# Kernel optimization log

Measured on AMD Instinct MI355X. Metric: run time of the kernel, lower is better.

Reference implementation:

```python
import jax, jax.numpy as jnp
import numpy as np

BOUNDS = (0, 256, 384, 448, 512)  # rot_idx, trans_idx, angle_idx, embedding_dim
SCALES = [1, 2, 4, 8, 16, 32, 64]  # 2**i for i in range(scales+1), scales=6


def _pairwise_dist(q, e):
    # q: [M, C] queries, e: [K, C] codebook; per-segment squared dist / seg_dim, summed
    d = jnp.zeros((q.shape[0], e.shape[0]), dtype=q.dtype)
    for s, t in zip(BOUNDS[:-1], BOUNDS[1:]):
        qs, es = q[:, s:t], e[:, s:t]
        d = d + (jnp.sum(qs * qs, axis=1, keepdims=True)
                 + jnp.sum(es * es, axis=1)
                 - 2.0 * qs @ es.T) / (t - s)
    return d


def _elem_dist(q, k):
    # q, k: [B, C, N]; elementwise per-segment squared distance / seg_dim -> [B, N]
    d = 0.0
    for s, t in zip(BOUNDS[:-1], BOUNDS[1:]):
        diff = q[:, s:t] - k[:, s:t]
        d = d + jnp.sum(diff * diff, axis=1) / (t - s)
    return d


def _downsample_area(f, pn):
    # f: [B, C, N], pn divides N -> block-mean pooling (torch 'area')
    B, C, N = f.shape
    return f.reshape(B, C, pn, N // pn).mean(axis=-1)


def _upsample_linear(h, N):
    # h: [B, C, pn] -> [B, C, N], torch mode='linear', align_corners=False
    pn = h.shape[-1]
    src = (jnp.arange(N, dtype=jnp.float32) + 0.5) * (pn / N) - 0.5
    src = jnp.clip(src, 0.0, pn - 1)
    i0 = jnp.floor(src).astype(jnp.int32)
    i1 = jnp.minimum(i0 + 1, pn - 1)
    w = (src - i0).astype(h.dtype)
    return h[..., i0] * (1.0 - w) + h[..., i1] * w


def setup_inputs() -> dict:
    key = jax.random.key(0)
    k1, k2, k3 = jax.random.split(key, 3)
    C = 512
    f_BNC = jax.random.normal(k1, (1024, 64, C), dtype=jnp.float32)
    base = jax.random.normal(k2, (2048, C), dtype=jnp.float32)
    proj_W = jax.random.normal(k3, (C, C), dtype=jnp.float32) / np.sqrt(C)
    return {"f_BNC": f_BNC, "base": base, "proj_W": proj_W}


def reference(f_BNC, base, proj_W):
    embedding = base @ proj_W.T              # update_embedding(): proj(base)
    emb_ng = jax.lax.stop_gradient(embedding)
    f_BCN = jnp.transpose(f_BNC, (0, 2, 1))  # [B, C, N]
    B, C, N = f_BCN.shape
    f_no_grad = jax.lax.stop_gradient(f_BCN)
    f_rest = f_no_grad
    f_hat = jnp.zeros_like(f_rest)
    commit = jnp.zeros((B, N), dtype=f_BCN.dtype)
    qlat = jnp.zeros((B, N), dtype=f_BCN.dtype)
    for pn in SCALES:
        rest_NC = jnp.transpose(_downsample_area(f_rest, pn), (0, 2, 1)).reshape(-1, C)
        d = _pairwise_dist(jax.lax.stop_gradient(rest_NC), emb_ng)  # [B*pn, K]
        idx = jnp.argmin(d, axis=1)
        h_NC = embedding[idx]                                        # gather (grad -> codebook)
        h_BCn = jnp.transpose(h_NC.reshape(B, pn, C), (0, 2, 1))
        h_BCN = _upsample_linear(h_BCn, N)
        f_hat = f_hat + h_BCN
        f_rest = f_rest - h_BCN
        commit = commit + 0.25 * _elem_dist(jax.lax.stop_gradient(f_hat), f_BCN)
        qlat = qlat + _elem_dist(f_hat, f_no_grad)
    SN = float(len(SCALES))
    commit = commit / SN
    qlat = qlat / SN
    f_hat_st = jax.lax.stop_gradient(f_hat) - f_no_grad + f_BCN  # straight-through
    return (jnp.transpose(f_hat_st, (0, 2, 1)), commit, qlat)
```

## Files before the change

kernel.cpp:

```cpp
#include <hip/hip_runtime.h>

typedef __attribute__((ext_vector_type(8))) _Float16 f16x8;
typedef __attribute__((ext_vector_type(4))) float f32x4;

#define B_    1024
#define C_    512
#define NCODE 2048
#define NTOT  (B_ * 64 * C_)
#define BN_   (B_ * 64)
#define DELTA 6e-3f

__device__ __forceinline__ float wseg(int k) {
    return k < 256 ? (1.0f / 256.0f) : (k < 384 ? (1.0f / 128.0f) : (1.0f / 64.0f));
}

__device__ __forceinline__ unsigned packkey(float s, int code) {
    unsigned u = __float_as_uint(s);
    u = (u & 0x80000000u) ? ~u : (u | 0x80000000u);
    return (u & 0xFFFFF800u) | (unsigned)code;
}
__device__ __forceinline__ float unpk(unsigned k) {
    unsigned us = k & 0xFFFFF800u;
    return (us & 0x80000000u) ? __uint_as_float(us ^ 0x80000000u) : __uint_as_float(~us);
}

__global__ __launch_bounds__(256) void k_gemm_e(const float* __restrict__ A,
                                                const float* __restrict__ Bm,
                                                float* __restrict__ E) {
    __shared__ float As[16][68];
    __shared__ float Bs[16][68];
    int tid = threadIdx.x;
    int m0 = blockIdx.x * 64, n0 = blockIdx.y * 64;
    float acc[4][4] = {};
    int tx = tid & 15, ty = tid >> 4;
    int kk = tid & 15, rr = tid >> 4;
    for (int k0 = 0; k0 < 512; k0 += 16) {
        #pragma unroll
        for (int i = 0; i < 4; ++i) {
            As[kk][rr + i * 16] = A[(m0 + rr + i * 16) * 512 + k0 + kk];
            Bs[kk][rr + i * 16] = Bm[(n0 + rr + i * 16) * 512 + k0 + kk];
        }
        __syncthreads();
        #pragma unroll
        for (int k = 0; k < 16; ++k) {
            float4 a = *(const float4*)&As[k][ty * 4];
            float4 b = *(const float4*)&Bs[k][tx * 4];
            #pragma unroll
            for (int i = 0; i < 4; ++i) {
                float av = ((const float*)&a)[i];
                acc[i][0] = fmaf(av, b.x, acc[i][0]);
                acc[i][1] = fmaf(av, b.y, acc[i][1]);
                acc[i][2] = fmaf(av, b.z, acc[i][2]);
                acc[i][3] = fmaf(av, b.w, acc[i][3]);
            }
        }
        __syncthreads();
    }
    #pragma unroll
    for (int i = 0; i < 4; ++i)
        #pragma unroll
        for (int j = 0; j < 4; ++j)
            E[(m0 + ty * 4 + i) * 512 + n0 + tx * 4 + j] = acc[i][j];
}

__global__ void k_wek16(const float* __restrict__ E, _Float16* __restrict__ wk) {
    int tid = blockIdx.x * 256 + threadIdx.x;
    int k = tid & 511;
    wk[tid] = (_Float16)(E[tid] * wseg(k));
}

__global__ void k_enorm(const float* __restrict__ E, float* __restrict__ enorm) {
    int c = blockIdx.x * 256 + threadIdx.x;
    float s = 0.0f;
    for (int k = 0; k < 512; ++k) {
        float v = E[c * 512 + k];
        s = fmaf(wseg(k) * v, v, s);
    }
    enorm[c] = s;
}

__global__ __launch_bounds__(256) void k_down0(const float* __restrict__ f,
                                               _Float16* __restrict__ q16,
                                               float* __restrict__ qf) {
    int b = blockIdx.x, t = threadIdx.x;
    const float* src = f + (size_t)b * 64 * 512;
    float s0 = 0.f, s1 = 0.f;
    for (int n = 0; n < 64; ++n) {
        s0 += src[n * 512 + t];
        s1 += src[n * 512 + t + 256];
    }
    s0 *= (1.0f / 64.0f); s1 *= (1.0f / 64.0f);
    q16[(size_t)b * 512 + t] = (_Float16)s0;
    q16[(size_t)b * 512 + t + 256] = (_Float16)s1;
    qf[(size_t)b * 512 + t] = s0;
    qf[(size_t)b * 512 + t + 256] = s1;
}

#define GLL2(gp, loff) __builtin_amdgcn_global_load_lds( \
    (const __attribute__((address_space(1))) unsigned int*)(gp), \
    (__attribute__((address_space(3))) unsigned int*)(smem + (loff)), 16, 0, 0)

__global__ __launch_bounds__(512, 2) void k_score_256(
        const _Float16* __restrict__ q16, const _Float16* __restrict__ wek,
        const float* __restrict__ enorm, float4* __restrict__ partial) {
    extern __shared__ char smem[];
    int tid = threadIdx.x;
    int x = blockIdx.x;
    int bx = (x >> 3) & 7;
    int g  = (x & 7) + ((x >> 6) << 3);
    int m0 = g * 256, n0 = bx * 256;

    int lane = tid & 63, wave = tid >> 6;
    int wm = wave >> 2, wn = wave & 3;
    int lx = lane & 15, cg = lane >> 4;

    int r2s = tid >> 3, sl = tid & 7;
    int us = sl ^ (r2s & 7);
    int cs = us & 3;
    int rws = r2s + ((us >> 2) << 6);
    const _Float16* srcA0 = q16 + (size_t)(m0 + rws) * 512 + cs * 8;
    const _Float16* srcA1 = q16 + (size_t)(m0 + 128 + rws) * 512 + cs * 8;
    const _Float16* srcB0 = wek + (size_t)(n0 + rws) * 512 + cs * 8;
    const _Float16* srcB1 = wek + (size_t)(n0 + 128 + rws) * 512 + cs * 8;

    #define STG_A(BUF, RH, KT) { const _Float16* s_ = ((RH) ? srcA1 : srcA0) + (KT) * 64; \
        GLL2(s_,      (BUF) * 65536 +     0 + (RH) * 8192 + tid * 16); \
        GLL2(s_ + 32, (BUF) * 65536 + 16384 + (RH) * 8192 + tid * 16); }
    #define STG_B(BUF, RH, KT) { const _Float16* s_ = ((RH) ? srcB1 : srcB0) + (KT) * 64; \
        GLL2(s_,      (BUF) * 65536 + 32768 + (RH) * 8192 + tid * 16); \
        GLL2(s_ + 32, (BUF) * 65536 + 49152 + (RH) * 8192 + tid * 16); }

    int Aoff[8];
    #pragma unroll
    for (int fi = 0; fi < 8; ++fi) {
        int rA = fi * 16 + lx;
        Aoff[fi] = wm * 8192 + (rA & 63) * 128 +
                   (((((rA >> 6) & 1) << 2) + cg) ^ (rA & 7)) * 16;
    }
    int Boff[4];
    #pragma unroll
    for (int fj = 0; fj < 4; ++fj) {
        int br = wn * 64 + fj * 16 + lx;
        int rB = br & 127;
        Boff[fj] = 32768 + (br >> 7) * 8192 + (rB & 63) * 128 +
                   (((((rB >> 6) & 1) << 2) + cg) ^ (rB & 7)) * 16;
    }

    f32x4 acc[8][4];
    #pragma unroll
    for (int i = 0; i < 8; ++i)
        #pragma unroll
        for (int j = 0; j < 4; ++j)
            acc[i][j] = (f32x4){0.f, 0.f, 0.f, 0.f};

    f16x8 bf00, bf01, bf10, bf11, bf20, bf21, bf30, bf31;
    #define LDB(BUF) \
        bf00 = *(const f16x8*)(smem + (BUF) * 65536 +         Boff[0]); \
        bf01 = *(const f16x8*)(smem + (BUF) * 65536 + 16384 + Boff[0]); \
        bf10 = *(const f16x8*)(smem + (BUF) * 65536 +         Boff[1]); \
        bf11 = *(const f16x8*)(smem + (BUF) * 65536 + 16384 + Boff[1]); \
        bf20 = *(const f16x8*)(smem + (BUF) * 65536 +         Boff[2]); \
        bf21 = *(const f16x8*)(smem + (BUF) * 65536 + 16384 + Boff[2]); \
        bf30 = *(const f16x8*)(smem + (BUF) * 65536 +         Boff[3]); \
        bf31 = *(const f16x8*)(smem + (BUF) * 65536 + 16384 + Boff[3]);

    #define MF(a, b, c) __builtin_amdgcn_mfma_f32_16x16x32_f16(a, b, c, 0, 0, 0)
    #define PH(BUF, F0, STAGE, VMW) { \
        f16x8 aA0 = *(const f16x8*)(smem + (BUF) * 65536 +         Aoff[F0]); \
        f16x8 aA1 = *(const f16x8*)(smem + (BUF) * 65536 + 16384 + Aoff[F0]); \
        f16x8 aB0 = *(const f16x8*)(smem + (BUF) * 65536 +         Aoff[(F0) + 1]); \
        f16x8 aB1 = *(const f16x8*)(smem + (BUF) * 65536 + 16384 + Aoff[(F0) + 1]); \
        STAGE; VMW; \
        __builtin_amdgcn_s_barrier(); \
        __builtin_amdgcn_s_setprio(1); \
        acc[F0][0] = MF(aA0, bf00, acc[F0][0]); acc[F0][0] = MF(aA1, bf01, acc[F0][0]); \
        acc[F0][1] = MF(aA0, bf10, acc[F0][1]); acc[F0][1] = MF(aA1, bf11, acc[F0][1]); \
        acc[F0][2] = MF(aA0, bf20, acc[F0][2]); acc[F0][2] = MF(aA1, bf21, acc[F0][2]); \
        acc[F0][3] = MF(aA0, bf30, acc[F0][3]); acc[F0][3] = MF(aA1, bf31, acc[F0][3]); \
        acc[(F0)+1][0] = MF(aB0, bf00, acc[(F0)+1][0]); acc[(F0)+1][0] = MF(aB1, bf01, acc[(F0)+1][0]); \
        acc[(F0)+1][1] = MF(aB0, bf10, acc[(F0)+1][1]); acc[(F0)+1][1] = MF(aB1, bf11, acc[(F0)+1][1]); \
        acc[(F0)+1][2] = MF(aB0, bf20, acc[(F0)+1][2]); acc[(F0)+1][2] = MF(aB1, bf21, acc[(F0)+1][2]); \
        acc[(F0)+1][3] = MF(aB0, bf30, acc[(F0)+1][3]); acc[(F0)+1][3] = MF(aB1, bf31, acc[(F0)+1][3]); \
        __builtin_amdgcn_s_setprio(0); \
        __builtin_amdgcn_s_barrier(); \
    }

    STG_A(0, 0, 0); STG_A(0, 1, 0); STG_B(0, 0, 0); STG_B(0, 1, 0);
    STG_B(1, 0, 1); STG_B(1, 1, 1); STG_A(1, 0, 1);
    asm volatile("s_waitcnt vmcnt(6)" ::: "memory");
    __builtin_amdgcn_s_barrier();

    #pragma unroll
    for (int it = 0; it < 4; ++it) {
        const int t0 = 2 * it, t1 = 2 * it + 1;
        LDB(0);
        PH(0, 0, STG_A(1, 1, t1), );
        PH(0, 2, if (it < 3) STG_B(0, 0, t0 + 2), );
        PH(0, 4, if (it < 3) STG_B(0, 1, t0 + 2), );
        PH(0, 6, if (it < 3) STG_A(0, 0, t0 + 2),
                 if (it < 3) { asm volatile("s_waitcnt vmcnt(6)" ::: "memory"); }
                 else        { asm volatile("s_waitcnt vmcnt(0)" ::: "memory"); });
        LDB(1);
        PH(1, 0, if (it < 3) STG_A(0, 1, t0 + 2), );
        PH(1, 2, if (it < 3) STG_B(1, 0, t0 + 3), );
        PH(1, 4, if (it < 3) STG_B(1, 1, t0 + 3), );
        PH(1, 6, if (it < 3) STG_A(1, 0, t0 + 3),
                 if (it < 3) { asm volatile("s_waitcnt vmcnt(6)" ::: "memory"); }
                 else        { asm volatile("s_waitcnt vmcnt(0)" ::: "memory"); });
    }

    float en[4];
    #pragma unroll
    for (int fj = 0; fj < 4; ++fj) en[fj] = enorm[n0 + wn * 64 + fj * 16 + lx];

    #pragma unroll
    for (int fi = 0; fi < 8; ++fi) {
        #pragma unroll
        for (int rr = 0; rr < 4; ++rr) {
            unsigned a1 = 0xFFFFFFFFu, a2 = 0xFFFFFFFFu;
            #pragma unroll
            for (int fj = 0; fj < 4; ++fj) {
                float s = fmaf(-2.0f, acc[fi][fj][rr], en[fj]);
                unsigned key = packkey(s, n0 + wn * 64 + fj * 16 + lx);
                if (key < a1) { a2 = a1; a1 = key; }
                else if (key < a2) a2 = key;
            }
            #pragma unroll
            for (int d = 1; d < 16; d <<= 1) {
                unsigned b1 = (unsigned)__shfl_xor((int)a1, d);
                unsigned b2 = (unsigned)__shfl_xor((int)a2, d);
                if (b1 < a1) { a2 = min(a1, b2); a1 = b1; }
                else a2 = min(a2, b1);
            }
            if (lx == 0) {
                int row = m0 + wm * 128 + fi * 16 + cg * 4 + rr;
                partial[(size_t)row * 32 + (bx * 4 + wn)] =
                    make_float4(unpk(a1), __int_as_float((int)(a1 & 2047u)),
                                unpk(a2), __int_as_float((int)(a2 & 2047u)));
            }
        }
    }
    #undef STG_A
    #undef STG_B
    #undef LDB
    #undef PH
    #undef MF
}

__global__ __launch_bounds__(256) void k_score_f16(
        const _Float16* __restrict__ q16, const _Float16* __restrict__ wek,
        const float* __restrict__ enorm, float4* __restrict__ partial) {
    __shared__ __align__(16) char smem[37376];
    float*  ensh = (float*)(smem + 32768);
    float4* bb   = (float4*)(smem + 33280);

    int tid = threadIdx.x;
    int x = blockIdx.x;
    int bx = (x >> 3) & 15;
    int g  = (x & 7) + ((x >> 7) << 3);
    int m0 = g * 128, n0 = bx * 128;
    if (tid < 128) ensh[tid] = enorm[n0 + tid];

    int lane = tid & 63, wave = tid >> 6;
    int wrow = (wave & 1) * 64, wcol = (wave >> 1) * 64;
    int lx = lane & 15, cg = lane >> 4;

    int u = (tid & 7) ^ ((tid >> 3) & 7);
    int chunk = u & 3;
    int rhi = (u >> 2) << 6;
    int r0 = (tid >> 3) + rhi;
    int r1 = 32 + (tid >> 3) + rhi;
    const _Float16* gqa0 = q16 + (size_t)(m0 + r0) * 512 + chunk * 8;
    const _Float16* gqa1 = q16 + (size_t)(m0 + r1) * 512 + chunk * 8;
    const _Float16* gwb0 = wek + (size_t)(n0 + r0) * 512 + chunk * 8;
    const _Float16* gwb1 = wek + (size_t)(n0 + r1) * 512 + chunk * 8;

    auto stage = [&](int buf, int k0) {
        GLL2(gqa0 + k0, buf * 16384 + tid * 16);
        GLL2(gqa1 + k0, buf * 16384 + 4096 + tid * 16);
        GLL2(gwb0 + k0, buf * 16384 + 8192 + tid * 16);
        GLL2(gwb1 + k0, buf * 16384 + 12288 + tid * 16);
    };

    f32x4 acc[4][4];
    #pragma unroll
    for (int i = 0; i < 4; ++i)
        #pragma unroll
        for (int j = 0; j < 4; ++j)
            acc[i][j] = (f32x4){0.f, 0.f, 0.f, 0.f};

    int swzA = (((wrow >> 6) * 4 + cg) ^ (lx & 7)) * 16;
    int swzB = (((wcol >> 6) * 4 + cg) ^ (lx & 7)) * 16;
    int abase = lx * 128 + swzA;
    int bbase = 8192 + lx * 128 + swzB;

    stage(0, 0);
    __syncthreads();

    #pragma unroll
    for (int ks = 0; ks < 16; ++ks) {
        int p = ks & 1;
        if (ks < 15) stage(p ^ 1, (ks + 1) * 32);
        f16x8 af[4], bf[4];
        #pragma unroll
        for (int i = 0; i < 4; ++i) {
            af[i] = *(const f16x8*)(smem + p * 16384 + abase + i * 2048);
            bf[i] = *(const f16x8*)(smem + p * 16384 + bbase + i * 2048);
        }
        #pragma unroll
        for (int i = 0; i < 4; ++i)
            #pragma unroll
            for (int j = 0; j < 4; ++j)
                acc[i][j] = __builtin_amdgcn_mfma_f32_16x16x32_f16(af[i], bf[j], acc[i][j], 0, 0, 0);
        __syncthreads();
    }

    #pragma unroll
    for (int fi = 0; fi < 4; ++fi) {
        #pragma unroll
        for (int r = 0; r < 4; ++r) {
            float v1 = INFINITY, v2 = INFINITY; int i1 = NCODE, i2 = NCODE;
            #pragma unroll
            for (int fj = 0; fj < 4; ++fj) {
                int nl = wcol + fj * 16 + lx;
                float s = ensh[nl] - 2.0f * acc[fi][fj][r];
                int code = n0 + nl;
                if (s < v1) { v2 = v1; i2 = i1; v1 = s; i1 = code; }
                else if (s < v2) { v2 = s; i2 = code; }
            }
            #pragma unroll
            for (int d = 1; d < 16; d <<= 1) {
                float ov1 = __shfl_xor(v1, d), ov2 = __shfl_xor(v2, d);
                int oi1 = __shfl_xor(i1, d), oi2 = __shfl_xor(i2, d);
                if (ov1 < v1) {
                    if (v1 < ov2) { v2 = v1; i2 = i1; } else { v2 = ov2; i2 = oi2; }
                    v1 = ov1; i1 = oi1;
                } else if (ov1 < v2) { v2 = ov1; i2 = oi1; }
            }
            if (lx == 0) {
                int row = wrow + fi * 16 + cg * 4 + r;
                bb[row * 2 + (wave >> 1)] = make_float4(v1, __int_as_float(i1),
                                                        v2, __int_as_float(i2));
            }
        }
    }
    __syncthreads();
    if (tid < 128) {
        float4 A4 = bb[tid * 2], C4 = bb[tid * 2 + 1];
        float v1, v2; int i1, i2;
        if (A4.x <= C4.x) {
            v1 = A4.x; i1 = __float_as_int(A4.y);
            if (A4.z <= C4.x) { v2 = A4.z; i2 = __float_as_int(A4.w); }
            else { v2 = C4.x; i2 = __float_as_int(C4.y); }
        } else {
            v1 = C4.x; i1 = __float_as_int(C4.y);
            if (C4.z <= A4.x) { v2 = C4.z; i2 = __float_as_int(C4.w); }
            else { v2 = A4.x; i2 = __float_as_int(A4.y); }
        }
        partial[(size_t)(m0 + tid) * 16 + bx] =
            make_float4(v1, __int_as_float(i1), v2, __int_as_float(i2));
    }
}

__global__ __launch_bounds__(256) void k_rescue(
        const float4* __restrict__ partial, const float* __restrict__ qf,
        const float* __restrict__ E, const float* __restrict__ enorm,
        int* __restrict__ idxb, int nslots) {
    int wid = (blockIdx.x * 256 + threadIdx.x) >> 6;
    int lane = threadIdx.x & 63;
    float4 p;
    if (lane < nslots) p = partial[(size_t)wid * nslots + lane];
    else p = make_float4(INFINITY, __int_as_float(NCODE), INFINITY, __int_as_float(NCODE));
    float bv = p.x;
    #pragma unroll
    for (int d = 1; d < 64; d <<= 1) bv = fminf(bv, __shfl_xor(bv, d));
    float thresh = bv + DELTA;
    unsigned long long m1 = __ballot(lane < nslots && p.x <= thresh);
    unsigned long long m2 = __ballot(lane < nslots && p.z <= thresh);
    const float* q = qf + (size_t)wid * 512 + lane * 8;
    float4 q0 = *(const float4*)q;
    float4 q1 = *(const float4*)(q + 4);
    float w = wseg(lane * 8);
    float qw0 = q0.x * w, qw1 = q0.y * w, qw2 = q0.z * w, qw3 = q0.w * w;
    float qw4 = q1.x * w, qw5 = q1.y * w, qw6 = q1.z * w, qw7 = q1.w * w;
    float bs = INFINITY; int bi = NCODE;
    while (m1 | m2) {
        int ci;
        if (m1) {
            int src = __ffsll((long long)m1) - 1; m1 &= m1 - 1;
            ci = __shfl(__float_as_int(p.y), src);
        } else {
            int src = __ffsll((long long)m2) - 1; m2 &= m2 - 1;
            ci = __shfl(__float_as_int(p.w), src);
        }
        const float* e = E + (size_t)ci * 512 + lane * 8;
        float4 e0 = *(const float4*)e;
        float4 e1 = *(const float4*)(e + 4);
        float a = 0.f;
        a = fmaf(qw0, e0.x, a); a = fmaf(qw1, e0.y, a);
        a = fmaf(qw2, e0.z, a); a = fmaf(qw3, e0.w, a);
        a = fmaf(qw4, e1.x, a); a = fmaf(qw5, e1.y, a);
        a = fmaf(qw6, e1.z, a); a = fmaf(qw7, e1.w, a);
        #pragma unroll
        for (int d = 1; d < 64; d <<= 1) a += __shfl_xor(a, d);
        float s = enorm[ci] - 2.0f * a;
        if (s < bs || (s == bs && ci < bi)) { bs = s; bi = ci; }
    }
    if (lane == 0) idxb[wid] = bi;
}

__global__ __launch_bounds__(256) void k_update(
        const float* __restrict__ E, const int* __restrict__ idx,
        const float* __restrict__ f, float* __restrict__ rest,
        float* __restrict__ dacc, _Float16* __restrict__ q16n,
        float* __restrict__ qf32n, int pn, int sn, int mode) {
    int t = threadIdx.x;
    int pn_next = 1 << sn;
    int r = 64 >> sn;
    int b = blockIdx.x >> sn;
    int chunk = blockIdx.x & (pn_next - 1);
    float w0 = wseg(t), w1 = wseg(t + 256);
    float macc0 = 0.f, macc1 = 0.f;
    float pscale = (float)pn * (1.0f / 64.0f);
    __shared__ float redw[4];
    for (int ri = 0; ri < r; ++ri) {
        int n = chunk * r + ri;
        int row = (b << 6) + n;
        float srcp = fminf(fmaxf((n + 0.5f) * pscale - 0.5f, 0.0f), (float)(pn - 1));
        int i0 = (int)floorf(srcp);
        int i1 = min(i0 + 1, pn - 1);
        float wl = srcp - (float)i0;
        int cc0 = idx[b * pn + i0];
        int cc1 = idx[b * pn + i1];
        const float* e0 = E + (size_t)cc0 * 512;
        const float* e1 = E + (size_t)cc1 * 512;
        const float* rs = (mode & 1) ? f + (size_t)row * 512 : rest + (size_t)row * 512;
        float s = 0.f;
        {
            float h = (1.0f - wl) * e0[t] + wl * e1[t];
            float v = rs[t] - h;
            rest[(size_t)row * 512 + t] = (mode & 2) ? (f[(size_t)row * 512 + t] - v) : v;
            s = fmaf(w0 * v, v, s);
            macc0 += v;
        }
        {
            int c = t + 256;
            float h = (1.0f - wl) * e0[c] + wl * e1[c];
            float v = rs[c] - h;
            rest[(size_t)row * 512 + c] = (mode & 2) ? (f[(size_t)row * 512 + c] - v) : v;
            s = fmaf(w1 * v, v, s);
            macc1 += v;
        }
        #pragma unroll
        for (int d = 1; d < 64; d <<= 1) s += __shfl_xor(s, d);
        if ((t & 63) == 0) redw[t >> 6] = s;
        __syncthreads();
        if (t == 0) {
            float tot = redw[0] + redw[1] + redw[2] + redw[3];
            dacc[row] = (mode & 1) ? tot : dacc[row] + tot;
        }
        __syncthreads();
    }
    if (!(mode & 2)) {
        float inv = 1.0f / (float)r;
        size_t qrow = ((size_t)b << sn) + chunk;
        float m0v = macc0 * inv, m1v = macc1 * inv;
        q16n[qrow * 512 + t] = (_Float16)m0v;
        q16n[qrow * 512 + t + 256] = (_Float16)m1v;
        if (mode & 4) {
            qf32n[qrow * 512 + t] = m0v;
            qf32n[qrow * 512 + t + 256] = m1v;
        }
    }
}

__global__ void k_out12(const float* __restrict__ dacc, float* __restrict__ out) {
    int i = blockIdx.x * 256 + threadIdx.x;
    float d = dacc[i];
    out[i] = d * (0.25f / 7.0f);
    out[BN_ + i] = d * (1.0f / 7.0f);
}

extern "C" void kernel_launch(void* const* d_in, const int* in_sizes, int n_in,
                              void* d_out, int out_size, void* d_ws, size_t ws_size,
                              hipStream_t stream) {
    const float* f    = (const float*)d_in[0];
    const float* base = (const float*)d_in[1];
    const float* W    = (const float*)d_in[2];
    float* out = (float*)d_out;
    float* rest = out;

    char* ws = (char*)d_ws;
    float*     E      = (float*)ws;     ws += (size_t)NCODE * 512 * 4;
    _Float16*  wek16  = (_Float16*)ws;  ws += (size_t)NCODE * 512 * 2;
    _Float16*  q16a   = (_Float16*)ws;  ws += (size_t)32768 * 512 * 2;
    char*      big64  = ws;             ws += (size_t)65536 * 512 * 2;
    float4*    partS  = (float4*)ws;    ws += (size_t)32768 * 32 * 16;
    float*     dacc   = (float*)ws;     ws += (size_t)BN_ * 4;
    int*       idxb   = (int*)ws;       ws += (size_t)BN_ * 4;
    float*     enorm  = (float*)ws;     ws += (size_t)NCODE * 4;

    k_gemm_e<<<dim3(NCODE / 64, 512 / 64), 256, 0, stream>>>(base, W, E);
    k_wek16<<<(NCODE * 512) / 256, 256, 0, stream>>>(E, wek16);
    k_enorm<<<NCODE / 256, 256, 0, stream>>>(E, enorm);
    k_down0<<<B_, 256, 0, stream>>>(f, q16a, (float*)big64);

    const int scales[7] = {1, 2, 4, 8, 16, 32, 64};
    for (int si = 0; si < 7; ++si) {
        int pn = scales[si];
        int M = 1024 * pn;
        const _Float16* q16s = (pn == 64) ? (const _Float16*)big64 : q16a;
        const float*    qfs  = (pn == 64) ? rest : (const float*)big64;

        if (pn >= 8) {
            float4* part = (pn == 64) ? (float4*)q16a : partS;
            k_score_256<<<8 * (M / 256), 512, 131072, stream>>>(q16s, wek16, enorm, part);
            k_rescue<<<M / 4, 256, 0, stream>>>(part, qfs, E, enorm, idxb, 32);
        } else {
            k_score_f16<<<16 * (M / 128), 256, 0, stream>>>(q16s, wek16, enorm, partS);
            k_rescue<<<M / 4, 256, 0, stream>>>(partS, qfs, E, enorm, idxb, 16);
        }

        int pn_next = (si == 6) ? 64 : pn * 2;
        int sn = 0; while ((1 << sn) != pn_next) ++sn;
        int mode = (si == 0 ? 1 : 0) | (si == 6 ? 2 : 0) | ((si <= 4) ? 4 : 0);
        _Float16* q16n = (pn_next == 64) ? (_Float16*)big64 : q16a;
        k_update<<<1024 * pn_next, 256, 0, stream>>>(E, idxb, f, rest, dacc,
                                                     q16n, (float*)big64, pn, sn, mode);
    }

    k_out12<<<BN_ / 256, 256, 0, stream>>>(dacc, out + NTOT);
}
```

Measured before the change: 1.117 ms.

## Software-pipeline LDS fragment reads ahead of MFMAs in 256-tile score kernel

Restructures the main loop of the 256x256 fp16 score GEMM so that A and B fragments for the next phase are read from LDS into double-buffered registers while the current phase's MFMAs run. It also cuts barriers from two per phase to one and reorders the global-to-LDS staging and waitcnt points. Launch bounds drop from two blocks per CU to one, giving more registers for the extra fragment buffers at the cost of occupancy. The risk is more register pressure and less latency hiding from a second resident block.

```diff
diff --git a/kernel.cpp b/kernel.cpp
--- a/kernel.cpp
+++ b/kernel.cpp
@@ -100,7 +100,7 @@
     (const __attribute__((address_space(1))) unsigned int*)(gp), \
     (__attribute__((address_space(3))) unsigned int*)(smem + (loff)), 16, 0, 0)
 
-__global__ __launch_bounds__(512, 2) void k_score_256(
+__global__ __launch_bounds__(512, 1) void k_score_256(
         const _Float16* __restrict__ q16, const _Float16* __restrict__ wek,
         const float* __restrict__ enorm, float4* __restrict__ partial) {
     extern __shared__ char smem[];
@@ -153,60 +153,64 @@
         for (int j = 0; j < 4; ++j)
             acc[i][j] = (f32x4){0.f, 0.f, 0.f, 0.f};
 
-    f16x8 bf00, bf01, bf10, bf11, bf20, bf21, bf30, bf31;
-    #define LDB(BUF) \
-        bf00 = *(const f16x8*)(smem + (BUF) * 65536 +         Boff[0]); \
-        bf01 = *(const f16x8*)(smem + (BUF) * 65536 + 16384 + Boff[0]); \
-        bf10 = *(const f16x8*)(smem + (BUF) * 65536 +         Boff[1]); \
-        bf11 = *(const f16x8*)(smem + (BUF) * 65536 + 16384 + Boff[1]); \
-        bf20 = *(const f16x8*)(smem + (BUF) * 65536 +         Boff[2]); \
-        bf21 = *(const f16x8*)(smem + (BUF) * 65536 + 16384 + Boff[2]); \
-        bf30 = *(const f16x8*)(smem + (BUF) * 65536 +         Boff[3]); \
-        bf31 = *(const f16x8*)(smem + (BUF) * 65536 + 16384 + Boff[3]);
+    f16x8 aR[2][4];
+    f16x8 bR[2][8];
+
+    #define RDA(X, BUF, F) { \
+        aR[X][0] = *(const f16x8*)(smem + (BUF) * 65536 +         Aoff[F]); \
+        aR[X][1] = *(const f16x8*)(smem + (BUF) * 65536 + 16384 + Aoff[F]); \
+        aR[X][2] = *(const f16x8*)(smem + (BUF) * 65536 +         Aoff[(F) + 1]); \
+        aR[X][3] = *(const f16x8*)(smem + (BUF) * 65536 + 16384 + Aoff[(F) + 1]); }
+    #define RDB(P) { \
+        _Pragma("unroll") \
+        for (int fj = 0; fj < 4; ++fj) { \
+            bR[P][2 * fj]     = *(const f16x8*)(smem + (P) * 65536 +         Boff[fj]); \
+            bR[P][2 * fj + 1] = *(const f16x8*)(smem + (P) * 65536 + 16384 + Boff[fj]); } }
 
     #define MF(a, b, c) __builtin_amdgcn_mfma_f32_16x16x32_f16(a, b, c, 0, 0, 0)
-    #define PH(BUF, F0, STAGE, VMW) { \
-        f16x8 aA0 = *(const f16x8*)(smem + (BUF) * 65536 +         Aoff[F0]); \
-        f16x8 aA1 = *(const f16x8*)(smem + (BUF) * 65536 + 16384 + Aoff[F0]); \
-        f16x8 aB0 = *(const f16x8*)(smem + (BUF) * 65536 +         Aoff[(F0) + 1]); \
-        f16x8 aB1 = *(const f16x8*)(smem + (BUF) * 65536 + 16384 + Aoff[(F0) + 1]); \
-        STAGE; VMW; \
-        __builtin_amdgcn_s_barrier(); \
-        __builtin_amdgcn_s_setprio(1); \
-        acc[F0][0] = MF(aA0, bf00, acc[F0][0]); acc[F0][0] = MF(aA1, bf01, acc[F0][0]); \
-        acc[F0][1] = MF(aA0, bf10, acc[F0][1]); acc[F0][1] = MF(aA1, bf11, acc[F0][1]); \
-        acc[F0][2] = MF(aA0, bf20, acc[F0][2]); acc[F0][2] = MF(aA1, bf21, acc[F0][2]); \
-        acc[F0][3] = MF(aA0, bf30, acc[F0][3]); acc[F0][3] = MF(aA1, bf31, acc[F0][3]); \
-        acc[(F0)+1][0] = MF(aB0, bf00, acc[(F0)+1][0]); acc[(F0)+1][0] = MF(aB1, bf01, acc[(F0)+1][0]); \
-        acc[(F0)+1][1] = MF(aB0, bf10, acc[(F0)+1][1]); acc[(F0)+1][1] = MF(aB1, bf11, acc[(F0)+1][1]); \
-        acc[(F0)+1][2] = MF(aB0, bf20, acc[(F0)+1][2]); acc[(F0)+1][2] = MF(aB1, bf21, acc[(F0)+1][2]); \
-        acc[(F0)+1][3] = MF(aB0, bf30, acc[(F0)+1][3]); acc[(F0)+1][3] = MF(aB1, bf31, acc[(F0)+1][3]); \
-        __builtin_amdgcn_s_setprio(0); \
-        __builtin_amdgcn_s_barrier(); \
-    }
+    #define MFMA16(X, P, F0) { \
+        _Pragma("unroll") \
+        for (int fj = 0; fj < 4; ++fj) { \
+            acc[F0][fj]       = MF(aR[X][0], bR[P][2 * fj],     acc[F0][fj]); \
+            acc[F0][fj]       = MF(aR[X][1], bR[P][2 * fj + 1], acc[F0][fj]); \
+            acc[(F0) + 1][fj] = MF(aR[X][2], bR[P][2 * fj],     acc[(F0) + 1][fj]); \
+            acc[(F0) + 1][fj] = MF(aR[X][3], bR[P][2 * fj + 1], acc[(F0) + 1][fj]); } }
 
     STG_A(0, 0, 0); STG_A(0, 1, 0); STG_B(0, 0, 0); STG_B(0, 1, 0);
     STG_B(1, 0, 1); STG_B(1, 1, 1); STG_A(1, 0, 1);
     asm volatile("s_waitcnt vmcnt(6)" ::: "memory");
     __builtin_amdgcn_s_barrier();
-
-    #pragma unroll
-    for (int it = 0; it < 4; ++it) {
-        const int t0 = 2 * it, t1 = 2 * it + 1;
-        LDB(0);
-        PH(0, 0, STG_A(1, 1, t1), );
-        PH(0, 2, if (it < 3) STG_B(0, 0, t0 + 2), );
-        PH(0, 4, if (it < 3) STG_B(0, 1, t0 + 2), );
-        PH(0, 6, if (it < 3) STG_A(0, 0, t0 + 2),
-                 if (it < 3) { asm volatile("s_waitcnt vmcnt(6)" ::: "memory"); }
-                 else        { asm volatile("s_waitcnt vmcnt(0)" ::: "memory"); });
-        LDB(1);
-        PH(1, 0, if (it < 3) STG_A(0, 1, t0 + 2), );
-        PH(1, 2, if (it < 3) STG_B(1, 0, t0 + 3), );
-        PH(1, 4, if (it < 3) STG_B(1, 1, t0 + 3), );
-        PH(1, 6, if (it < 3) STG_A(1, 0, t0 + 3),
-                 if (it < 3) { asm volatile("s_waitcnt vmcnt(6)" ::: "memory"); }
-                 else        { asm volatile("s_waitcnt vmcnt(0)" ::: "memory"); });
+    RDB(0); RDA(0, 0, 0);
+
+    #pragma unroll
+    for (int t = 0; t < 8; ++t) {
+        const int p = t & 1, q = p ^ 1;
+        __builtin_amdgcn_s_barrier();
+        RDA(1, p, 2);
+        if (t < 7) STG_A(q, 1, t + 1);
+        __builtin_amdgcn_s_setprio(1);
+        MFMA16(0, p, 0);
+        __builtin_amdgcn_s_setprio(0);
+        __builtin_amdgcn_s_barrier();
+        RDA(0, p, 4);
+        if (t < 6) STG_B(p, 0, t + 2);
+        __builtin_amdgcn_s_setprio(1);
+        MFMA16(1, p, 2);
+        __builtin_amdgcn_s_setprio(0);
+        __builtin_amdgcn_s_barrier();
+        RDA(1, p, 6);
+        if (t < 6) STG_B(p, 1, t + 2);
+        __builtin_amdgcn_s_setprio(1);
+        MFMA16(0, p, 4);
+        __builtin_amdgcn_s_setprio(0);
+        if (t < 6)      { asm volatile("s_waitcnt vmcnt(4)" ::: "memory"); }
+        else if (t == 6){ asm volatile("s_waitcnt vmcnt(0)" ::: "memory"); }
+        __builtin_amdgcn_s_barrier();
+        if (t < 7) { RDB(q); RDA(0, q, 0); }
+        if (t < 6) STG_A(p, 0, t + 2);
+        __builtin_amdgcn_s_setprio(1);
+        MFMA16(1, p, 6);
+        __builtin_amdgcn_s_setprio(0);
     }
 
     float en[4];
@@ -242,8 +246,9 @@
     }
     #undef STG_A
     #undef STG_B
-    #undef LDB
-    #undef PH
+    #undef RDA
+    #undef RDB
+    #undef MFMA16
     #undef MF
 }
 
```

Result: slower. 1.302 ms (+16.5%).
